# Optimization experiments

Measured on AMD Instinct MI355X. Metric: run time of the kernel, lower is better.

Reference implementation:

```python
import jax, jax.numpy as jnp
import numpy as np

ALPHA = 0.2  # LeakyReLU negative slope

def setup_inputs() -> dict:
    key = jax.random.key(0)
    k1, k2, k3, k4 = jax.random.split(key, 4)
    B, N, D = 20000, 32, 128
    return {
        "self_vectors": jax.random.normal(k1, (B, D), dtype=jnp.float32),
        "neighbor_vector": jax.random.normal(k2, (B, N, D), dtype=jnp.float32),
        "w": jax.random.normal(k3, (D, D), dtype=jnp.float32) * (1.0 / np.sqrt(D)),
        "q": jax.random.normal(k4, (D, 1), dtype=jnp.float32) * (1.0 / np.sqrt(D)),
    }

def reference(self_vectors, neighbor_vector, w, q):
    # neighbor_message: [B, N, D]
    neighbor_message = jnp.einsum('bnd,de->bne', neighbor_vector, w)
    # broadcast self vector over neighbor axis: [B, 1, D] * [B, N, D]
    attn_feat = self_vectors[:, None, :] * neighbor_message
    attn_feat = jnp.where(attn_feat >= 0, attn_feat, ALPHA * attn_feat)  # LeakyReLU
    attn_score = jnp.einsum('bnd,d->bn', attn_feat, q[:, 0])  # [B, N]
    alpha = jax.nn.softmax(attn_score, axis=-1)  # softmax over neighbors
    # weighted sum over neighbors: [B, D]
    return jnp.einsum('bn,bnd->bd', alpha, neighbor_message)
```

## Files before the change

### kernel.cpp

```cpp
#include <hip/hip_runtime.h>
#include <hip/hip_bf16.h>


#define NNBR 32
#define DIM  128
#define BPB  8

typedef short  short8 __attribute__((ext_vector_type(8)));
typedef float  f32x4  __attribute__((ext_vector_type(4)));

__device__ __forceinline__ ushort f2bf(float x) {
    uint u = __float_as_uint(x);
    u += 0x7FFFu + ((u >> 16) & 1u);
    return (ushort)(u >> 16);
}

__global__ __launch_bounds__(256) void hete_agg_kernel(
    const float* __restrict__ selfv,
    const float* __restrict__ nbr,
    const float* __restrict__ w,
    const float* __restrict__ q,
    float* __restrict__ out)
{
    __shared__ ushort nbs[NNBR * DIM];
    __shared__ float  msg[NNBR * (DIM + 1)];
    __shared__ float  sfl[DIM];
    __shared__ float  qs[DIM];
    __shared__ float  scoreL[NNBR];
    __shared__ float  alphaL[NNBR];

    const int tid = threadIdx.x;
    const int l   = tid & 63;
    const int wid = tid >> 6;
    const int mt  = wid & 1;
    const int ng  = wid >> 1;
    const int lr  = l & 15;
    const int lk  = l >> 4;

    if (tid < 32) {
        float4 v = *(const float4*)(q + tid * 4);
        *(float4*)(qs + tid * 4) = v;
    }

    short8 bfrag[4][4];
    {
        const int colE = ng * 64 + lr;
        #pragma unroll
        for (int nt = 0; nt < 4; ++nt) {
            #pragma unroll
            for (int kk = 0; kk < 4; ++kk) {
                short8 f;
                #pragma unroll
                for (int i = 0; i < 8; ++i) {
                    int krow = kk * 32 + lk * 8 + i;
                    f[i] = (short)f2bf(w[krow * DIM + colE + nt * 16]);
                }
                bfrag[nt][kk] = f;
            }
        }
    }

    for (int bi = 0; bi < BPB; ++bi) {
        const int b = blockIdx.x * BPB + bi;

        {
            const float4* src = (const float4*)(nbr + (size_t)b * NNBR * DIM);
            #pragma unroll
            for (int it = 0; it < 4; ++it) {
                int f   = tid + it * 256;
                int row = f >> 5;
                int c4  = (f & 31) * 4;
                float4 v = src[f];
                ushort4 bv;
                bv.x = f2bf(v.x); bv.y = f2bf(v.y);
                bv.z = f2bf(v.z); bv.w = f2bf(v.w);
                int col = c4 ^ ((row & 7) << 3);
                *(ushort4*)(&nbs[row * DIM + col]) = bv;
            }
            if (tid < 32) {
                float4 v = *(const float4*)(selfv + (size_t)b * DIM + tid * 4);
                *(float4*)(sfl + tid * 4) = v;
            }
        }
        __syncthreads();

        f32x4 acc[4] = {};
        #pragma unroll
        for (int kk = 0; kk < 4; ++kk) {
            int row = mt * 16 + lr;
            int col = (kk * 32 + lk * 8) ^ ((row & 7) << 3);
            short8 a = *(const short8*)(&nbs[row * DIM + col]);
            #pragma unroll
            for (int nt = 0; nt < 4; ++nt)
                acc[nt] = __builtin_amdgcn_mfma_f32_16x16x32_bf16(a, bfrag[nt][kk], acc[nt], 0, 0, 0);
        }

        #pragma unroll
        for (int nt = 0; nt < 4; ++nt) {
            #pragma unroll
            for (int r = 0; r < 4; ++r) {
                int row = mt * 16 + lk * 4 + r;
                int col = ng * 64 + nt * 16 + lr;
                msg[row * (DIM + 1) + col] = acc[nt][r];
            }
        }
        __syncthreads();

        {
            int n  = tid >> 3;
            int d0 = (tid & 7) * 16;
            float p = 0.f;
            #pragma unroll
            for (int j = 0; j < 16; ++j) {
                int d = d0 + j;
                float m = msg[n * (DIM + 1) + d];
                float a = sfl[d] * m;
                a = (a >= 0.f) ? a : 0.2f * a;
                p += a * qs[d];
            }
            #pragma unroll
            for (int off = 1; off < 8; off <<= 1) p += __shfl_xor(p, off);
            if ((tid & 7) == 0) scoreL[n] = p;
        }
        __syncthreads();

        if (tid < 32) {
            float s = scoreL[tid];
            float m = s;
            #pragma unroll
            for (int off = 1; off < 32; off <<= 1) m = fmaxf(m, __shfl_xor(m, off));
            float e = __expf(s - m);
            float sum = e;
            #pragma unroll
            for (int off = 1; off < 32; off <<= 1) sum += __shfl_xor(sum, off);
            alphaL[tid] = e / sum;
        }
        __syncthreads();

        if (tid < DIM) {
            float o = 0.f;
            #pragma unroll
            for (int n = 0; n < NNBR; ++n)
                o += alphaL[n] * msg[n * (DIM + 1) + tid];
            out[(size_t)b * DIM + tid] = o;
        }
        __syncthreads();
    }
}

extern "C" void kernel_launch(void* const* d_in, const int* in_sizes, int n_in,
                              void* d_out, int out_size, void* d_ws, size_t ws_size,
                              hipStream_t stream) {
    const float* selfv = (const float*)d_in[0];
    const float* nbr   = (const float*)d_in[1];
    const float* w     = (const float*)d_in[2];
    const float* q     = (const float*)d_in[3];
    float* out = (float*)d_out;

    const int B = in_sizes[0] / DIM;
    const int nblocks = B / BPB;
    hete_agg_kernel<<<nblocks, 256, 0, stream>>>(selfv, nbr, w, q, out);
}
```

Baseline: 506.5 us.

## Rewrite as persistent double-buffered kernel with async global-to-LDS loads

Replaces the per-8-batch block design with a persistent grid of 512 blocks of 512 threads. Each block handles about 39 batches, W is converted to bf16 once into LDS, and neighbor tiles are double-buffered via global_load_lds with explicit waitcnt and barriers. Scores, softmax and the weighted sum stay in registers using shuffles instead of an fp32 message matrix in LDS, which cuts barriers and LDS traffic. The batch partition (512 blocks, 39/40 batches each) is hardcoded for B=20000 and ignores in_sizes. Hand-written vmcnt counting is fragile.

```diff
diff --git a/kernel.cpp b/kernel.cpp
--- a/kernel.cpp
+++ b/kernel.cpp
@@ -4,147 +4,178 @@
 
 #define NNBR 32
 #define DIM  128
-#define BPB  8
 
 typedef short  short8 __attribute__((ext_vector_type(8)));
 typedef float  f32x4  __attribute__((ext_vector_type(4)));
 
-__device__ __forceinline__ ushort f2bf(float x) {
-    uint u = __float_as_uint(x);
-    u += 0x7FFFu + ((u >> 16) & 1u);
-    return (ushort)(u >> 16);
+#define GLL(gsrc, ldst) \
+    __builtin_amdgcn_global_load_lds((const __attribute__((address_space(1))) void*)(gsrc), \
+                                     (__attribute__((address_space(3))) void*)(ldst), 16, 0, 0)
+
+__device__ __forceinline__ short8 cvt_bf8(float4 a, float4 b) {
+    __hip_bfloat162 p0 = __float22bfloat162_rn(make_float2(a.x, a.y));
+    __hip_bfloat162 p1 = __float22bfloat162_rn(make_float2(a.z, a.w));
+    __hip_bfloat162 p2 = __float22bfloat162_rn(make_float2(b.x, b.y));
+    __hip_bfloat162 p3 = __float22bfloat162_rn(make_float2(b.z, b.w));
+    union { __hip_bfloat162 h[4]; short8 s; } u;
+    u.h[0] = p0; u.h[1] = p1; u.h[2] = p2; u.h[3] = p3;
+    return u.s;
 }
 
-__global__ __launch_bounds__(256) void hete_agg_kernel(
+__global__ __launch_bounds__(512, 4) void hete_agg_kernel(
     const float* __restrict__ selfv,
     const float* __restrict__ nbr,
     const float* __restrict__ w,
     const float* __restrict__ q,
     float* __restrict__ out)
 {
-    __shared__ ushort nbs[NNBR * DIM];
-    __shared__ float  msg[NNBR * (DIM + 1)];
-    __shared__ float  sfl[DIM];
-    __shared__ float  qs[DIM];
-    __shared__ float  scoreL[NNBR];
-    __shared__ float  alphaL[NNBR];
+    __shared__ ushort wt[DIM * DIM];
+    __shared__ float  nbuf[2 * NNBR * DIM];
+    __shared__ float  scoreP[8 * NNBR];
 
     const int tid = threadIdx.x;
     const int l   = tid & 63;
-    const int wid = tid >> 6;
-    const int mt  = wid & 1;
-    const int ng  = wid >> 1;
+    const int wv  = tid >> 6;
     const int lr  = l & 15;
     const int lk  = l >> 4;
+    const int ecol = wv * 16 + lr;
 
-    if (tid < 32) {
-        float4 v = *(const float4*)(q + tid * 4);
-        *(float4*)(qs + tid * 4) = v;
+    for (int it = 0; it < 8; ++it) {
+        int g  = tid + it * 512;
+        int d  = g >> 5;
+        int e4 = (g & 31) * 4;
+        float4 v = *(const float4*)(w + g * 4);
+        float xs[4] = {v.x, v.y, v.z, v.w};
+        #pragma unroll
+        for (int j = 0; j < 4; ++j) {
+            int e = e4 + j;
+            uint u = __float_as_uint(xs[j]);
+            u += 0x7FFFu + ((u >> 16) & 1u);
+            wt[e * DIM + (d ^ ((e & 7) << 3))] = (ushort)(u >> 16);
+        }
+    }
+    const float qv  = q[ecol];
+    const float q02 = 0.2f * qv;
+
+    __syncthreads();
+
+    const int bid = blockIdx.x;
+    const int b0  = bid * 39 + (bid < 32 ? bid : 32);
+    const int cnt = 39 + (bid < 32 ? 1 : 0);
+
+    int srcoff0, srcoff1;
+    {
+        int L0 = (wv)*1024 + l*16;
+        int r0 = L0 >> 9;
+        srcoff0 = r0 * 512 + ((L0 & 511) ^ ((r0 & 7) << 4));
+        int L1 = (8 + wv)*1024 + l*16;
+        int r1 = L1 >> 9;
+        srcoff1 = r1 * 512 + ((L1 & 511) ^ ((r1 & 7) << 4));
     }
 
-    short8 bfrag[4][4];
+    float selfA = selfv[(size_t)b0 * DIM + ecol];
+    float selfB = selfv[(size_t)(b0 + 1) * DIM + ecol];
     {
-        const int colE = ng * 64 + lr;
+        const char* g0 = (const char*)nbr + (size_t)b0 * 16384;
+        const char* g1 = (const char*)nbr + (size_t)(b0 + 1) * 16384;
+        char* lb0 = (char*)nbuf + wv * 1024;
+        char* lb1 = (char*)nbuf + 16384 + wv * 1024;
+        GLL(g0 + srcoff0, lb0);
+        GLL(g0 + srcoff1, lb0 + 8192);
+        GLL(g1 + srcoff0, lb1);
+        GLL(g1 + srcoff1, lb1 + 8192);
+    }
+
+    for (int t = 0; t < cnt; ++t) {
+        const int cur = t & 1;
+
+        if (t == 0) { asm volatile("s_waitcnt vmcnt(2)" ::: "memory"); }
+        else        { asm volatile("s_waitcnt vmcnt(3)" ::: "memory"); }
+        __builtin_amdgcn_s_barrier();
+        __builtin_amdgcn_sched_barrier(0);
+
+        const char* nb = (const char*)nbuf + cur * 16384;
+        f32x4 acc0 = {0.f, 0.f, 0.f, 0.f};
+        f32x4 acc1 = {0.f, 0.f, 0.f, 0.f};
         #pragma unroll
-        for (int nt = 0; nt < 4; ++nt) {
+        for (int kk = 0; kk < 4; ++kk) {
+            const int bcol = (kk * 32 + lk * 8) ^ ((ecol & 7) << 3);
+            short8 bf = *(const short8*)(&wt[ecol * DIM + bcol]);
             #pragma unroll
-            for (int kk = 0; kk < 4; ++kk) {
-                short8 f;
-                #pragma unroll
-                for (int i = 0; i < 8; ++i) {
-                    int krow = kk * 32 + lk * 8 + i;
-                    f[i] = (short)f2bf(w[krow * DIM + colE + nt * 16]);
-                }
-                bfrag[nt][kk] = f;
+            for (int mt = 0; mt < 2; ++mt) {
+                const int row = mt * 16 + lr;
+                const int sw  = (row & 7) << 4;
+                const int byt = kk * 128 + lk * 32;
+                float4 f0 = *(const float4*)(nb + row * 512 + ((byt)      ^ sw));
+                float4 f1 = *(const float4*)(nb + row * 512 + ((byt + 16) ^ sw));
+                short8 af = cvt_bf8(f0, f1);
+                if (mt == 0) acc0 = __builtin_amdgcn_mfma_f32_16x16x32_bf16(af, bf, acc0, 0, 0, 0);
+                else         acc1 = __builtin_amdgcn_mfma_f32_16x16x32_bf16(af, bf, acc1, 0, 0, 0);
             }
         }
-    }
 
-    for (int bi = 0; bi < BPB; ++bi) {
-        const int b = blockIdx.x * BPB + bi;
+        float sc0[4], sc1[4];
+        #pragma unroll
+        for (int r = 0; r < 4; ++r) {
+            float x0 = selfA * acc0[r];
+            sc0[r] = (x0 >= 0.f ? qv : q02) * x0;
+            float x1 = selfA * acc1[r];
+            sc1[r] = (x1 >= 0.f ? qv : q02) * x1;
+        }
+        #pragma unroll
+        for (int off = 1; off < 16; off <<= 1) {
+            #pragma unroll
+            for (int r = 0; r < 4; ++r) {
+                sc0[r] += __shfl_xor(sc0[r], off);
+                sc1[r] += __shfl_xor(sc1[r], off);
+            }
+        }
+        if (lr == 0) {
+            #pragma unroll
+            for (int r = 0; r < 4; ++r) {
+                scoreP[wv * 32 + lk * 4 + r]      = sc0[r];
+                scoreP[wv * 32 + 16 + lk * 4 + r] = sc1[r];
+            }
+        }
+
+        asm volatile("s_waitcnt lgkmcnt(0)" ::: "memory");
+        __builtin_amdgcn_s_barrier();
+        __builtin_amdgcn_sched_barrier(0);
 
         {
-            const float4* src = (const float4*)(nbr + (size_t)b * NNBR * DIM);
-            #pragma unroll
-            for (int it = 0; it < 4; ++it) {
-                int f   = tid + it * 256;
-                int row = f >> 5;
-                int c4  = (f & 31) * 4;
-                float4 v = src[f];
-                ushort4 bv;
-                bv.x = f2bf(v.x); bv.y = f2bf(v.y);
-                bv.z = f2bf(v.z); bv.w = f2bf(v.w);
-                int col = c4 ^ ((row & 7) << 3);
-                *(ushort4*)(&nbs[row * DIM + col]) = bv;
-            }
-            if (tid < 32) {
-                float4 v = *(const float4*)(selfv + (size_t)b * DIM + tid * 4);
-                *(float4*)(sfl + tid * 4) = v;
-            }
+            const int tn = (t + 2 < cnt) ? t + 2 : cnt - 1;
+            selfA = selfB;
+            selfB = selfv[(size_t)(b0 + tn) * DIM + ecol];
+            const char* gn = (const char*)nbr + (size_t)(b0 + tn) * 16384;
+            char* lbn = (char*)nbuf + cur * 16384 + wv * 1024;
+            GLL(gn + srcoff0, lbn);
+            GLL(gn + srcoff1, lbn + 8192);
         }
-        __syncthreads();
+        __builtin_amdgcn_sched_barrier(0);
 
-        f32x4 acc[4] = {};
+        const int n = l & 31;
+        float s = 0.f;
         #pragma unroll
-        for (int kk = 0; kk < 4; ++kk) {
-            int row = mt * 16 + lr;
-            int col = (kk * 32 + lk * 8) ^ ((row & 7) << 3);
-            short8 a = *(const short8*)(&nbs[row * DIM + col]);
-            #pragma unroll
-            for (int nt = 0; nt < 4; ++nt)
-                acc[nt] = __builtin_amdgcn_mfma_f32_16x16x32_bf16(a, bfrag[nt][kk], acc[nt], 0, 0, 0);
+        for (int w8 = 0; w8 < 8; ++w8) s += scoreP[w8 * 32 + n];
+        float mx = s;
+        #pragma unroll
+        for (int off = 1; off < 32; off <<= 1) mx = fmaxf(mx, __shfl_xor(mx, off));
+        float ee = __expf(s - mx);
+        float sm = ee;
+        #pragma unroll
+        for (int off = 1; off < 32; off <<= 1) sm += __shfl_xor(sm, off);
+        const float al = ee * __builtin_amdgcn_rcpf(sm);
+
+        float o = 0.f;
+        #pragma unroll
+        for (int r = 0; r < 4; ++r) {
+            float a0 = __shfl(al, lk * 4 + r);
+            float a1 = __shfl(al, 16 + lk * 4 + r);
+            o += a0 * acc0[r] + a1 * acc1[r];
         }
-
-        #pragma unroll
-        for (int nt = 0; nt < 4; ++nt) {
-            #pragma unroll
-            for (int r = 0; r < 4; ++r) {
-                int row = mt * 16 + lk * 4 + r;
-                int col = ng * 64 + nt * 16 + lr;
-                msg[row * (DIM + 1) + col] = acc[nt][r];
-            }
-        }
-        __syncthreads();
-
-        {
-            int n  = tid >> 3;
-            int d0 = (tid & 7) * 16;
-            float p = 0.f;
-            #pragma unroll
-            for (int j = 0; j < 16; ++j) {
-                int d = d0 + j;
-                float m = msg[n * (DIM + 1) + d];
-                float a = sfl[d] * m;
-                a = (a >= 0.f) ? a : 0.2f * a;
-                p += a * qs[d];
-            }
-            #pragma unroll
-            for (int off = 1; off < 8; off <<= 1) p += __shfl_xor(p, off);
-            if ((tid & 7) == 0) scoreL[n] = p;
-        }
-        __syncthreads();
-
-        if (tid < 32) {
-            float s = scoreL[tid];
-            float m = s;
-            #pragma unroll
-            for (int off = 1; off < 32; off <<= 1) m = fmaxf(m, __shfl_xor(m, off));
-            float e = __expf(s - m);
-            float sum = e;
-            #pragma unroll
-            for (int off = 1; off < 32; off <<= 1) sum += __shfl_xor(sum, off);
-            alphaL[tid] = e / sum;
-        }
-        __syncthreads();
-
-        if (tid < DIM) {
-            float o = 0.f;
-            #pragma unroll
-            for (int n = 0; n < NNBR; ++n)
-                o += alphaL[n] * msg[n * (DIM + 1) + tid];
-            out[(size_t)b * DIM + tid] = o;
-        }
-        __syncthreads();
+        o += __shfl_xor(o, 16);
+        o += __shfl_xor(o, 32);
+        if (l < 16) out[(size_t)(b0 + t) * DIM + wv * 16 + l] = o;
     }
 }
 
@@ -157,7 +188,5 @@
     const float* q     = (const float*)d_in[3];
     float* out = (float*)d_out;
 
-    const int B = in_sizes[0] / DIM;
-    const int nblocks = B / BPB;
-    hete_agg_kernel<<<nblocks, 256, 0, stream>>>(selfv, nbr, w, q, out);
+    hete_agg_kernel<<<512, 512, 0, stream>>>(selfv, nbr, w, q, out);
 }
```

New measurement: 504.0 us. Within noise of the previous version (-0.5%).

## Restructure to one batch per wavefront with register prefetch and persistent grid

Applied to the files above, without the earlier changes.

Rewrites the kernel so each wavefront handles a whole batch element entirely in registers. W is cached in shared memory as transposed, swizzled bf16, and the next batch's neighbor tile is prefetched into registers while the current one runs through MFMA. Scores, softmax and the weighted sum are done with lane shuffles, removing the shared-memory message buffer and all per-batch block barriers. The launch is hardcoded to 500 blocks and a fixed stride of 2000 over 10 iterations, so it only works for B=20000 and raises register pressure.

```diff
diff --git a/kernel.cpp b/kernel.cpp
--- a/kernel.cpp
+++ b/kernel.cpp
@@ -2,12 +2,10 @@
 #include <hip/hip_bf16.h>
 
 
-#define NNBR 32
-#define DIM  128
-#define BPB  8
+#define DIM 128
 
-typedef short  short8 __attribute__((ext_vector_type(8)));
-typedef float  f32x4  __attribute__((ext_vector_type(4)));
+typedef short short8 __attribute__((ext_vector_type(8)));
+typedef float f32x4  __attribute__((ext_vector_type(4)));
 
 __device__ __forceinline__ ushort f2bf(float x) {
     uint u = __float_as_uint(x);
@@ -15,136 +13,169 @@
     return (ushort)(u >> 16);
 }
 
-__global__ __launch_bounds__(256) void hete_agg_kernel(
+__device__ __forceinline__ short8 cvt_bf8(float4 a, float4 b) {
+    __hip_bfloat162 p0 = __float22bfloat162_rn(make_float2(a.x, a.y));
+    __hip_bfloat162 p1 = __float22bfloat162_rn(make_float2(a.z, a.w));
+    __hip_bfloat162 p2 = __float22bfloat162_rn(make_float2(b.x, b.y));
+    __hip_bfloat162 p3 = __float22bfloat162_rn(make_float2(b.z, b.w));
+    union { __hip_bfloat162 h[4]; short8 s; } u;
+    u.h[0] = p0; u.h[1] = p1; u.h[2] = p2; u.h[3] = p3;
+    return u.s;
+}
+
+__global__ __launch_bounds__(256, 2) void hete_agg_kernel(
     const float* __restrict__ selfv,
     const float* __restrict__ nbr,
     const float* __restrict__ w,
     const float* __restrict__ q,
     float* __restrict__ out)
 {
-    __shared__ ushort nbs[NNBR * DIM];
-    __shared__ float  msg[NNBR * (DIM + 1)];
-    __shared__ float  sfl[DIM];
-    __shared__ float  qs[DIM];
-    __shared__ float  scoreL[NNBR];
-    __shared__ float  alphaL[NNBR];
+    __shared__ ushort wt[DIM * DIM];
 
     const int tid = threadIdx.x;
+
+    #pragma unroll
+    for (int it = 0; it < 16; ++it) {
+        int g  = tid + it * 256;
+        int d  = g >> 5;
+        int e4 = (g & 31) * 4;
+        float4 v = *(const float4*)(w + (size_t)g * 4);
+        float xs[4] = {v.x, v.y, v.z, v.w};
+        #pragma unroll
+        for (int j = 0; j < 4; ++j) {
+            int e = e4 + j;
+            wt[e * DIM + (d ^ ((e & 7) << 3))] = f2bf(xs[j]);
+        }
+    }
+    __syncthreads();
+
     const int l   = tid & 63;
-    const int wid = tid >> 6;
-    const int mt  = wid & 1;
-    const int ng  = wid >> 1;
+    const int wv  = tid >> 6;
     const int lr  = l & 15;
     const int lk  = l >> 4;
+    const int wid = blockIdx.x * 4 + wv;
 
-    if (tid < 32) {
-        float4 v = *(const float4*)(q + tid * 4);
-        *(float4*)(qs + tid * 4) = v;
+    float qS[8];
+    #pragma unroll
+    for (int et = 0; et < 8; ++et) qS[et] = q[et * 16 + lr];
+
+    float4 st[16];
+    float  selfN[8], selfC[8];
+
+    {
+        const float* nb = nbr + (size_t)wid * (32 * DIM);
+        #pragma unroll
+        for (int mt = 0; mt < 2; ++mt)
+            #pragma unroll
+            for (int kk = 0; kk < 4; ++kk)
+                #pragma unroll
+                for (int c = 0; c < 2; ++c)
+                    st[mt * 8 + kk * 2 + c] =
+                        *(const float4*)(nb + (mt * 16 + lr) * DIM + kk * 32 + lk * 8 + c * 4);
+        #pragma unroll
+        for (int et = 0; et < 8; ++et)
+            selfN[et] = selfv[(size_t)wid * DIM + et * 16 + lr];
     }
 
-    short8 bfrag[4][4];
-    {
-        const int colE = ng * 64 + lr;
+    for (int t = 0; t < 10; ++t) {
+        const int b = wid + t * 2000;
+
+        short8 afrag[2][4];
         #pragma unroll
-        for (int nt = 0; nt < 4; ++nt) {
+        for (int mt = 0; mt < 2; ++mt)
             #pragma unroll
-            for (int kk = 0; kk < 4; ++kk) {
-                short8 f;
+            for (int kk = 0; kk < 4; ++kk)
+                afrag[mt][kk] = cvt_bf8(st[mt * 8 + kk * 2 + 0], st[mt * 8 + kk * 2 + 1]);
+        #pragma unroll
+        for (int et = 0; et < 8; ++et) selfC[et] = selfN[et];
+
+        {
+            const int bn = (t < 9) ? (b + 2000) : b;
+            const float* nb = nbr + (size_t)bn * (32 * DIM);
+            #pragma unroll
+            for (int mt = 0; mt < 2; ++mt)
                 #pragma unroll
-                for (int i = 0; i < 8; ++i) {
-                    int krow = kk * 32 + lk * 8 + i;
-                    f[i] = (short)f2bf(w[krow * DIM + colE + nt * 16]);
-                }
-                bfrag[nt][kk] = f;
+                for (int kk = 0; kk < 4; ++kk)
+                    #pragma unroll
+                    for (int c = 0; c < 2; ++c)
+                        st[mt * 8 + kk * 2 + c] =
+                            *(const float4*)(nb + (mt * 16 + lr) * DIM + kk * 32 + lk * 8 + c * 4);
+            #pragma unroll
+            for (int et = 0; et < 8; ++et)
+                selfN[et] = selfv[(size_t)bn * DIM + et * 16 + lr];
+        }
+
+        f32x4 acc[2][8] = {};
+        #pragma unroll
+        for (int kk = 0; kk < 4; ++kk) {
+            #pragma unroll
+            for (int et = 0; et < 8; ++et) {
+                const int e = et * 16 + lr;
+                short8 bf = *(const short8*)(&wt[e * DIM + ((kk * 32 + lk * 8) ^ ((e & 7) << 3))]);
+                acc[0][et] = __builtin_amdgcn_mfma_f32_16x16x32_bf16(afrag[0][kk], bf, acc[0][et], 0, 0, 0);
+                acc[1][et] = __builtin_amdgcn_mfma_f32_16x16x32_bf16(afrag[1][kk], bf, acc[1][et], 0, 0, 0);
             }
         }
-    }
 
-    for (int bi = 0; bi < BPB; ++bi) {
-        const int b = blockIdx.x * BPB + bi;
+        float sc[2][4];
+        #pragma unroll
+        for (int mt = 0; mt < 2; ++mt)
+            #pragma unroll
+            for (int r = 0; r < 4; ++r) {
+                float s = 0.f;
+                #pragma unroll
+                for (int et = 0; et < 8; ++et) {
+                    float x = selfC[et] * acc[mt][et][r];
+                    x = (x >= 0.f) ? x : 0.2f * x;
+                    s += x * qS[et];
+                }
+                sc[mt][r] = s;
+            }
+        #pragma unroll
+        for (int off = 1; off < 16; off <<= 1)
+            #pragma unroll
+            for (int mt = 0; mt < 2; ++mt)
+                #pragma unroll
+                for (int r = 0; r < 4; ++r)
+                    sc[mt][r] += __shfl_xor(sc[mt][r], off);
 
-        {
-            const float4* src = (const float4*)(nbr + (size_t)b * NNBR * DIM);
+        float mx = sc[0][0];
+        #pragma unroll
+        for (int mt = 0; mt < 2; ++mt)
             #pragma unroll
-            for (int it = 0; it < 4; ++it) {
-                int f   = tid + it * 256;
-                int row = f >> 5;
-                int c4  = (f & 31) * 4;
-                float4 v = src[f];
-                ushort4 bv;
-                bv.x = f2bf(v.x); bv.y = f2bf(v.y);
-                bv.z = f2bf(v.z); bv.w = f2bf(v.w);
-                int col = c4 ^ ((row & 7) << 3);
-                *(ushort4*)(&nbs[row * DIM + col]) = bv;
-            }
-            if (tid < 32) {
-                float4 v = *(const float4*)(selfv + (size_t)b * DIM + tid * 4);
-                *(float4*)(sfl + tid * 4) = v;
-            }
+            for (int r = 0; r < 4; ++r) mx = fmaxf(mx, sc[mt][r]);
+        mx = fmaxf(mx, __shfl_xor(mx, 16));
+        mx = fmaxf(mx, __shfl_xor(mx, 32));
+        float p[2][4], S = 0.f;
+        #pragma unroll
+        for (int mt = 0; mt < 2; ++mt)
+            #pragma unroll
+            for (int r = 0; r < 4; ++r) { p[mt][r] = __expf(sc[mt][r] - mx); S += p[mt][r]; }
+        S += __shfl_xor(S, 16);
+        S += __shfl_xor(S, 32);
+        const float inv = __builtin_amdgcn_rcpf(S);
+
+        float o[8];
+        #pragma unroll
+        for (int et = 0; et < 8; ++et) {
+            float v = 0.f;
+            #pragma unroll
+            for (int mt = 0; mt < 2; ++mt)
+                #pragma unroll
+                for (int r = 0; r < 4; ++r)
+                    v += p[mt][r] * acc[mt][et][r];
+            o[et] = v * inv;
         }
-        __syncthreads();
-
-        f32x4 acc[4] = {};
         #pragma unroll
-        for (int kk = 0; kk < 4; ++kk) {
-            int row = mt * 16 + lr;
-            int col = (kk * 32 + lk * 8) ^ ((row & 7) << 3);
-            short8 a = *(const short8*)(&nbs[row * DIM + col]);
-            #pragma unroll
-            for (int nt = 0; nt < 4; ++nt)
-                acc[nt] = __builtin_amdgcn_mfma_f32_16x16x32_bf16(a, bfrag[nt][kk], acc[nt], 0, 0, 0);
+        for (int et = 0; et < 8; ++et) {
+            o[et] += __shfl_xor(o[et], 16);
+            o[et] += __shfl_xor(o[et], 32);
         }
 
         #pragma unroll
-        for (int nt = 0; nt < 4; ++nt) {
-            #pragma unroll
-            for (int r = 0; r < 4; ++r) {
-                int row = mt * 16 + lk * 4 + r;
-                int col = ng * 64 + nt * 16 + lr;
-                msg[row * (DIM + 1) + col] = acc[nt][r];
-            }
-        }
-        __syncthreads();
-
-        {
-            int n  = tid >> 3;
-            int d0 = (tid & 7) * 16;
-            float p = 0.f;
-            #pragma unroll
-            for (int j = 0; j < 16; ++j) {
-                int d = d0 + j;
-                float m = msg[n * (DIM + 1) + d];
-                float a = sfl[d] * m;
-                a = (a >= 0.f) ? a : 0.2f * a;
-                p += a * qs[d];
-            }
-            #pragma unroll
-            for (int off = 1; off < 8; off <<= 1) p += __shfl_xor(p, off);
-            if ((tid & 7) == 0) scoreL[n] = p;
-        }
-        __syncthreads();
-
-        if (tid < 32) {
-            float s = scoreL[tid];
-            float m = s;
-            #pragma unroll
-            for (int off = 1; off < 32; off <<= 1) m = fmaxf(m, __shfl_xor(m, off));
-            float e = __expf(s - m);
-            float sum = e;
-            #pragma unroll
-            for (int off = 1; off < 32; off <<= 1) sum += __shfl_xor(sum, off);
-            alphaL[tid] = e / sum;
-        }
-        __syncthreads();
-
-        if (tid < DIM) {
-            float o = 0.f;
-            #pragma unroll
-            for (int n = 0; n < NNBR; ++n)
-                o += alphaL[n] * msg[n * (DIM + 1) + tid];
-            out[(size_t)b * DIM + tid] = o;
-        }
-        __syncthreads();
+        for (int et = 0; et < 8; ++et)
+            if (lk == (et >> 1))
+                out[(size_t)b * DIM + et * 16 + lr] = o[et];
     }
 }
 
@@ -157,7 +188,5 @@
     const float* q     = (const float*)d_in[3];
     float* out = (float*)d_out;
 
-    const int B = in_sizes[0] / DIM;
-    const int nblocks = B / BPB;
-    hete_agg_kernel<<<nblocks, 256, 0, stream>>>(selfv, nbr, w, q, out);
+    hete_agg_kernel<<<500, 256, 0, stream>>>(selfv, nbr, w, q, out);
 }
```

New measurement: 453.5 us. 10.5% less time.
